# Kernel tuning notes

Hardware: AMD Instinct MI355X
Metric: run time of the kernel (lower is better)

## Reference

```python
import jax, jax.numpy as jnp
import numpy as np

BS = 64; T = 96; C = 16; IN = 16; H = 256; NH = 8; DH = H // NH
NCLS = 4; L = T + NCLS; LAYERS = 4; GDEP = 2; EPS = 1e-5


def _ln(x, g, b):
    m = x.mean(-1, keepdims=True)
    v = ((x - m) ** 2).mean(-1, keepdims=True)
    return (x - m) / jnp.sqrt(v + EPS) * g + b


def _mask():
    # causal upper-triangular -inf mask; last NCLS rows (cls tokens) attend everywhere
    m = jnp.where(jnp.triu(jnp.ones((L, L), jnp.float32), 1) > 0, -jnp.inf, 0.0)
    return m.at[-NCLS:].set(0.0)


def _enc(h, mask, Wqkv, bqkv, Wo, bo, W1, b1, W2, b2, g1, be1, g2, be2):
    # post-norm TransformerEncoderLayer (torch default), dropout=0
    B = h.shape[0]
    qkv = h @ Wqkv.T + bqkv
    q, k, v = jnp.split(qkv, 3, axis=-1)
    sp = lambda t: t.reshape(B, L, NH, DH).transpose(0, 2, 1, 3)
    q, k, v = sp(q), sp(k), sp(v)
    s = jnp.einsum('bhqd,bhkd->bhqk', q, k) / np.float32(np.sqrt(DH)) + mask
    a = jax.nn.softmax(s, axis=-1)
    o = jnp.einsum('bhqk,bhkd->bhqd', a, v).transpose(0, 2, 1, 3).reshape(B, L, H)
    h = _ln(h + o @ Wo.T + bo, g1, be1)
    ff = jax.nn.relu(h @ W1.T + b1) @ W2.T + b2
    return _ln(h + ff, g2, be2)


def _mixprop(x, g, Wm, bm):
    # x: (bs, H, C, NCLS); MTGNN mixprop with alpha=0
    adj = g + jnp.eye(C, dtype=g.dtype)
    a = adj / adj.sum(1, keepdims=True)
    h = x
    outs = [x]
    for _ in range(GDEP):
        h = jnp.einsum('ncwl,vw->ncvl', h, a)
        outs.append(h)
    ho = jnp.concatenate(outs, axis=1)  # (bs, (GDEP+1)*H, C, NCLS)
    return jnp.einsum('ncwl,oc->nowl', ho, Wm) + bm[None, :, None, None]


def _forward(x, Wfc, bfc, cls_token, pos_emb, emb1, emb2, Wl1, bl1, Wl2, bl2,
             Wqkv, bqkv, Wo, bo, W1, b1, W2, b2, ln1g, ln1b, ln2g, ln2b,
             Wmlp, bmlp, Wd1, bd1, Wd2, bd2):
    bs = x.shape[0]
    h = x @ Wfc.T + bfc                                      # (bs,T,C,H)
    h = jnp.concatenate([h, jnp.broadcast_to(cls_token, (bs, NCLS, C, H))], axis=1)
    h = h + pos_emb[None]                                    # (bs,L,C,H)
    h = jnp.swapaxes(h, 1, 2).reshape(bs * C, L, H)
    mask = _mask()
    # graph_constructor (alpha=1)
    m1 = jnp.tanh(emb1 @ Wl1.T + bl1)
    m2 = jnp.tanh(emb2 @ Wl2.T + bl2)
    g = jax.nn.relu(jnp.tanh(m1 @ m2.T - m2 @ m1.T))         # (C,C)
    h = _enc(h, mask, Wqkv[0], bqkv[0], Wo[0], bo[0], W1[0], b1[0], W2[0], b2[0],
             ln1g[0], ln1b[0], ln2g[0], ln2b[0])
    for l in range(1, LAYERS):
        cls = h[:, -NCLS:].reshape(bs, C, NCLS, H).transpose(0, 3, 1, 2)  # (bs,H,C,NCLS)
        cls = _mixprop(cls, g, Wmlp[l - 1], bmlp[l - 1])
        cls = cls.transpose(0, 2, 3, 1).reshape(bs * C, NCLS, H)
        h = jnp.concatenate([h[:, :-NCLS], cls], axis=1)
        h = _enc(h, mask, Wqkv[l], bqkv[l], Wo[l], bo[l], W1[l], b1[l], W2[l], b2[l],
                 ln1g[l], ln1b[l], ln2g[l], ln2b[l])
    z = jnp.tanh(h[:, -NCLS:].reshape(bs, C * NCLS * H))
    z = jax.nn.gelu(z @ Wd1.T + bd1, approximate=False) @ Wd2.T + bd2
    return z[:, 0]


def setup_inputs() -> dict:
    key = jax.random.key(0)
    ks = iter(jax.random.split(key, 64))
    rn = lambda *s: jax.random.normal(next(ks), s, dtype=jnp.float32) * 0.05
    d = {}
    d['x'] = jax.random.normal(next(ks), (BS, T, C, IN), dtype=jnp.float32)
    d['p'] = jnp.zeros((BS,), jnp.float32)
    d['y'] = jnp.zeros((BS,), jnp.float32)
    d['Wfc'] = rn(H, IN); d['bfc'] = jnp.zeros((H,), jnp.float32)
    d['cls_token'] = rn(1, NCLS, C, H) * 20.0  # torch randn scale ~1
    d['pos_emb'] = rn(NCLS + T, C, H) * 20.0
    d['emb1'] = rn(C, H); d['emb2'] = rn(C, H)
    d['Wl1'] = rn(H, H); d['bl1'] = jnp.zeros((H,), jnp.float32)
    d['Wl2'] = rn(H, H); d['bl2'] = jnp.zeros((H,), jnp.float32)
    d['Wqkv'] = rn(LAYERS, 3 * H, H); d['bqkv'] = jnp.zeros((LAYERS, 3 * H), jnp.float32)
    d['Wo'] = rn(LAYERS, H, H); d['bo'] = jnp.zeros((LAYERS, H), jnp.float32)
    d['W1'] = rn(LAYERS, 4 * H, H); d['b1'] = jnp.zeros((LAYERS, 4 * H), jnp.float32)
    d['W2'] = rn(LAYERS, H, 4 * H); d['b2'] = jnp.zeros((LAYERS, H), jnp.float32)
    d['ln1g'] = jnp.ones((LAYERS, H), jnp.float32); d['ln1b'] = jnp.zeros((LAYERS, H), jnp.float32)
    d['ln2g'] = jnp.ones((LAYERS, H), jnp.float32); d['ln2b'] = jnp.zeros((LAYERS, H), jnp.float32)
    d['Wmlp'] = rn(LAYERS - 1, H, (GDEP + 1) * H); d['bmlp'] = jnp.zeros((LAYERS - 1, H), jnp.float32)
    d['Wd1'] = rn(H, NCLS * C * H); d['bd1'] = jnp.zeros((H,), jnp.float32)
    d['Wd2'] = rn(1, H); d['bd2'] = jnp.zeros((1,), jnp.float32)
    return d


def reference(x, p, y, Wfc, bfc, cls_token, pos_emb, emb1, emb2, Wl1, bl1, Wl2, bl2,
              Wqkv, bqkv, Wo, bo, W1, b1, W2, b2, ln1g, ln1b, ln2g, ln2b,
              Wmlp, bmlp, Wd1, bd1, Wd2, bd2):
    # p, y are unused by the original forward (kept for signature parity)
    return _forward(x, Wfc, bfc, cls_token, pos_emb, emb1, emb2, Wl1, bl1, Wl2, bl2,
                    Wqkv, bqkv, Wo, bo, W1, b1, W2, b2, ln1g, ln1b, ln2g, ln2b,
                    Wmlp, bmlp, Wd1, bd1, Wd2, bd2)
```

## Files before the change

kernel.cpp:

```cpp
#include <hip/hip_runtime.h>
#include <hip/hip_bf16.h>
#include <math.h>

typedef unsigned short u16;
typedef unsigned int   u32;
typedef __attribute__((ext_vector_type(8))) short short8;
typedef __attribute__((ext_vector_type(4))) float f32x4;

#define BSZ   64
#define TT    96
#define CCH   16
#define INDIM 16
#define HD    256
#define NHEAD 8
#define DHEAD 32
#define NCLS  4
#define LSEQ  100
#define NLAY  4
#define EPSV  1e-5f
#define BSEQ  (BSZ*CCH)
#define MTOK  (BSEQ*LSEQ)

__device__ __forceinline__ float bf2f(u16 x){ return __uint_as_float(((u32)x)<<16); }
__device__ __forceinline__ u16 f2bf(float f){
    u32 u = __float_as_uint(f);
    u32 r = (u + 0x7fffu + ((u>>16)&1u)) >> 16;
    return (u16)r;
}
__device__ __forceinline__ float lo16(u32 r){ return __uint_as_float(r<<16); }
__device__ __forceinline__ float hi16(u32 r){ return __uint_as_float(r&0xffff0000u); }

__device__ __forceinline__ u32 cvtpk(float lo, float hi){
    u32 r;
    asm("v_cvt_pk_bf16_f32 %0, %1, %2" : "=v"(r) : "v"(lo), "v"(hi));
    return r;
}

__device__ __forceinline__ void gload_lds16(const u16* g, u16* l){
    __builtin_amdgcn_global_load_lds(
        (const __attribute__((address_space(1))) unsigned int*)g,
        (__attribute__((address_space(3))) unsigned int*)l, 16, 0, 0);
}

__global__ __launch_bounds__(256)
void k_cvt(const float* __restrict__ src, u16* __restrict__ dst, int n)
{
    for (int i = blockIdx.x*256 + threadIdx.x; i < n; i += gridDim.x*256)
        dst[i] = f2bf(src[i]);
}

__global__ __launch_bounds__(256)
void k_embed(const float* __restrict__ x, const float* __restrict__ Wfc,
             const float* __restrict__ bfc, const float* __restrict__ cls,
             const float* __restrict__ pos, u16* __restrict__ h)
{
    int s = blockIdx.x;
    int n = s >> 4, c = s & 15;
    int hc = threadIdx.x;
    float wr[INDIM];
    #pragma unroll
    for (int i=0;i<INDIM;i++) wr[i] = Wfc[hc*INDIM + i];
    float bb = bfc[hc];
    for (int l=0; l<TT; l++){
        const float* xr = x + (size_t)((n*TT + l)*CCH + c)*INDIM;
        float acc = bb;
        #pragma unroll
        for (int i=0;i<INDIM;i++) acc += xr[i]*wr[i];
        acc += pos[(size_t)(l*CCH + c)*HD + hc];
        h[((size_t)s*LSEQ + l)*HD + hc] = f2bf(acc);
    }
    #pragma unroll
    for (int l=TT; l<LSEQ; l++){
        float v = cls[(size_t)((l-TT)*CCH + c)*HD + hc]
                + pos[(size_t)(l*CCH + c)*HD + hc];
        h[((size_t)s*LSEQ + l)*HD + hc] = f2bf(v);
    }
}

__global__ __launch_bounds__(256)
void k_graph_m(const float* __restrict__ emb, const float* __restrict__ Wl,
               const float* __restrict__ bl, float* __restrict__ m)
{
    int r = blockIdx.x, o = threadIdx.x;
    __shared__ float e[HD];
    e[o] = emb[r*HD + o];
    __syncthreads();
    const float* w = Wl + (size_t)o*HD;
    float acc = bl[o];
    for (int k=0;k<HD;k++) acc += e[k]*w[k];
    m[r*HD + o] = tanhf(acc);
}

__global__ __launch_bounds__(256)
void k_graph_a(const float* __restrict__ m1, const float* __restrict__ m2,
               float* __restrict__ a)
{
    int t = threadIdx.x; int v = t >> 4, w = t & 15;
    __shared__ float adj[16][17];
    float s1=0.f, s2=0.f;
    for (int k=0;k<HD;k++){
        s1 += m1[v*HD+k]*m2[w*HD+k];
        s2 += m2[v*HD+k]*m1[w*HD+k];
    }
    float g = tanhf(s1 - s2); g = g > 0.f ? g : 0.f;
    adj[v][w] = g + (v==w ? 1.f : 0.f);
    __syncthreads();
    float rs = 0.f;
    #pragma unroll
    for (int j=0;j<16;j++) rs += adj[v][j];
    a[t] = adj[v][w] / rs;
}

__global__ __launch_bounds__(256)
void k_gemmA(const u16* __restrict__ A, int lda,
             const u16* __restrict__ W, const float* __restrict__ bias,
             u16* __restrict__ C, int ldc, int K, int relu, int scat)
{
    __shared__ u16 As0[2][128*32], As1[2][128*32];
    __shared__ u16 Ws0[2][128*32], Ws1[2][128*32];
    int t = threadIdx.x;
    int lane = t & 63, w = t >> 6;
    int wm = (w & 1)*64, wn = (w >> 1)*64;
    int fr = lane & 15, quad = lane >> 4;
    size_t mb = (size_t)blockIdx.x * 128;
    int nb = blockIdx.y * 128;
    int srow = lane >> 2;
    int sslot = lane & 3;

    f32x4 acc[4][4] = {};

    auto STAGE = [&](int bb, int k0){
        #pragma unroll
        for (int i=0;i<2;i++){
            int r = w*32 + i*16 + srow;
            int cw = sslot ^ ((r>>1)&3);
            gload_lds16(&A[(mb + r)*(size_t)lda + k0      + cw*8], &As0[bb][(w*32 + i*16)*32]);
            gload_lds16(&A[(mb + r)*(size_t)lda + k0 + 32 + cw*8], &As1[bb][(w*32 + i*16)*32]);
            gload_lds16(&W[(size_t)(nb + r)*K   + k0      + cw*8], &Ws0[bb][(w*32 + i*16)*32]);
            gload_lds16(&W[(size_t)(nb + r)*K   + k0 + 32 + cw*8], &Ws1[bb][(w*32 + i*16)*32]);
        }
    };
    auto COMPUTE = [&](int bb){
        short8 af0[4], af1[4], bf0[4], bf1[4];
        #pragma unroll
        for (int mt=0; mt<4; mt++){
            int r = wm + mt*16 + fr;
            int sw = (quad ^ ((r>>1)&3)) << 3;
            af0[mt] = *(const short8*)&As0[bb][r*32 + sw];
            af1[mt] = *(const short8*)&As1[bb][r*32 + sw];
        }
        #pragma unroll
        for (int nt=0; nt<4; nt++){
            int r = wn + nt*16 + fr;
            int sw = (quad ^ ((r>>1)&3)) << 3;
            bf0[nt] = *(const short8*)&Ws0[bb][r*32 + sw];
            bf1[nt] = *(const short8*)&Ws1[bb][r*32 + sw];
        }
        #pragma unroll
        for (int mt=0; mt<4; mt++)
            #pragma unroll
            for (int nt=0; nt<4; nt++){
                acc[mt][nt] = __builtin_amdgcn_mfma_f32_16x16x32_bf16(
                    af0[mt], bf0[nt], acc[mt][nt], 0, 0, 0);
                acc[mt][nt] = __builtin_amdgcn_mfma_f32_16x16x32_bf16(
                    af1[mt], bf1[nt], acc[mt][nt], 0, 0, 0);
            }
    };

    const int nst = K >> 6;
    STAGE(0, 0);
    asm volatile("s_waitcnt vmcnt(0)" ::: "memory");
    __builtin_amdgcn_s_barrier();
    int b = 0;
    for (int ts = 0; ts < nst; ++ts){
        if (ts + 1 < nst) STAGE(b^1, (ts+1) << 6);
        COMPUTE(b);
        asm volatile("s_waitcnt vmcnt(0)" ::: "memory");
        __builtin_amdgcn_s_barrier();
        b ^= 1;
    }

    float bb4[4];
    #pragma unroll
    for (int nt=0; nt<4; nt++) bb4[nt] = bias[nb + wn + nt*16 + fr];
    #pragma unroll
    for (int mt=0; mt<4; mt++){
        size_t rbase = mb + wm + mt*16 + quad*4;
        size_t rows[4];
        #pragma unroll
        for (int r=0; r<4; r++){
            size_t rg = rbase + r;
            if (scat) rg = (rg >> 2)*LSEQ + TT + (rg & 3);
            rows[r] = rg*(size_t)ldc;
        }
        #pragma unroll
        for (int nt=0; nt<4; nt++){
            int col = nb + wn + nt*16 + fr;
            float v0 = acc[mt][nt][0] + bb4[nt];
            float v1 = acc[mt][nt][1] + bb4[nt];
            float v2 = acc[mt][nt][2] + bb4[nt];
            float v3 = acc[mt][nt][3] + bb4[nt];
            if (relu){
                v0 = v0 > 0.f ? v0 : 0.f;  v1 = v1 > 0.f ? v1 : 0.f;
                v2 = v2 > 0.f ? v2 : 0.f;  v3 = v3 > 0.f ? v3 : 0.f;
            }
            u32 p01 = cvtpk(v0, v1), p23 = cvtpk(v2, v3);
            C[rows[0] + col] = (u16)p01;
            C[rows[1] + col] = (u16)(p01 >> 16);
            C[rows[2] + col] = (u16)p23;
            C[rows[3] + col] = (u16)(p23 >> 16);
        }
    }
}

__global__ __launch_bounds__(256)
void k_gemmC(const u16* __restrict__ A, int lda, int K,
             const u16* __restrict__ W, const float* __restrict__ bias,
             u16* __restrict__ h, const float* __restrict__ gam,
             const float* __restrict__ bet, size_t row0)
{
    __shared__ u16 As0[2][64*32], As1[2][64*32];
    __shared__ u16 Ws0[2][256*32], Ws1[2][256*32];
    int t = threadIdx.x;
    int lane = t & 63, w = t >> 6;
    int fr = lane & 15, quad = lane >> 4;
    size_t mb = (size_t)blockIdx.x * 64;
    int srow = lane >> 2, sslot = lane & 3;

    f32x4 acc[4][4] = {};

    auto STAGE = [&](int bb, int k0){
        {
            int r = w*16 + srow;
            int cw = sslot ^ ((r>>1)&3);
            gload_lds16(&A[(mb + r)*(size_t)lda + k0      + cw*8], &As0[bb][(w*16)*32]);
            gload_lds16(&A[(mb + r)*(size_t)lda + k0 + 32 + cw*8], &As1[bb][(w*16)*32]);
        }
        #pragma unroll
        for (int i=0;i<4;i++){
            int r = w*64 + i*16 + srow;
            int cw = sslot ^ ((r>>1)&3);
            gload_lds16(&W[(size_t)r*K + k0      + cw*8], &Ws0[bb][(w*64 + i*16)*32]);
            gload_lds16(&W[(size_t)r*K + k0 + 32 + cw*8], &Ws1[bb][(w*64 + i*16)*32]);
        }
    };
    auto COMPUTE = [&](int bb){
        short8 af0[4], af1[4], bf0[4], bf1[4];
        #pragma unroll
        for (int mt=0; mt<4; mt++){
            int ra = mt*16 + fr;
            int swa = (quad ^ ((ra>>1)&3)) << 3;
            af0[mt] = *(const short8*)&As0[bb][ra*32 + swa];
            af1[mt] = *(const short8*)&As1[bb][ra*32 + swa];
        }
        #pragma unroll
        for (int nt=0; nt<4; nt++){
            int rb = w*64 + nt*16 + fr;
            int swb = (quad ^ ((rb>>1)&3)) << 3;
            bf0[nt] = *(const short8*)&Ws0[bb][rb*32 + swb];
            bf1[nt] = *(const short8*)&Ws1[bb][rb*32 + swb];
        }
        #pragma unroll
        for (int mt=0; mt<4; mt++)
            #pragma unroll
            for (int nt=0; nt<4; nt++){
                acc[mt][nt] = __builtin_amdgcn_mfma_f32_16x16x32_bf16(
                    af0[mt], bf0[nt], acc[mt][nt], 0, 0, 0);
                acc[mt][nt] = __builtin_amdgcn_mfma_f32_16x16x32_bf16(
                    af1[mt], bf1[nt], acc[mt][nt], 0, 0, 0);
            }
    };

    const int nst = K >> 6;
    STAGE(0, 0);
    asm volatile("s_waitcnt vmcnt(0)" ::: "memory");
    __builtin_amdgcn_s_barrier();
    int b = 0;
    for (int ts = 0; ts < nst; ++ts){
        if (ts + 1 < nst) STAGE(b^1, (ts+1) << 6);
        COMPUTE(b);
        asm volatile("s_waitcnt vmcnt(0)" ::: "memory");
        __builtin_amdgcn_s_barrier();
        b ^= 1;
    }

    float bb4[4], gg[4], be[4];
    #pragma unroll
    for (int nt=0; nt<4; nt++){
        int col = w*64 + nt*16 + fr;
        bb4[nt] = bias[col]; gg[nt] = gam[col]; be[nt] = bet[col];
    }
    #pragma unroll
    for (int mt=0; mt<4; mt++){
        #pragma unroll
        for (int r=0; r<4; r++){
            size_t row = row0 + mb + mt*16 + quad*4 + r;
            #pragma unroll
            for (int nt=0; nt<4; nt++)
                acc[mt][nt][r] += bb4[nt] + bf2f(h[row*HD + w*64 + nt*16 + fr]);
        }
    }
    __syncthreads();
    float* red  = (float*)As0;
    float* red2 = (float*)As1;
    float ps[4][4];
    #pragma unroll
    for (int mt=0; mt<4; mt++)
        #pragma unroll
        for (int r=0; r<4; r++){
            float s = acc[mt][0][r] + acc[mt][1][r] + acc[mt][2][r] + acc[mt][3][r];
            s += __shfl_xor(s,1,64); s += __shfl_xor(s,2,64);
            s += __shfl_xor(s,4,64); s += __shfl_xor(s,8,64);
            ps[mt][r] = s;
        }
    if (fr == 0){
        #pragma unroll
        for (int mt=0; mt<4; mt++)
            #pragma unroll
            for (int r=0; r<4; r++)
                red[w*64 + mt*16 + quad*4 + r] = ps[mt][r];
    }
    __syncthreads();
    float mean[4][4];
    #pragma unroll
    for (int mt=0; mt<4; mt++)
        #pragma unroll
        for (int r=0; r<4; r++){
            int rl = mt*16 + quad*4 + r;
            mean[mt][r] = (red[rl] + red[64+rl] + red[128+rl] + red[192+rl]) * (1.f/256.f);
            float s = 0.f;
            #pragma unroll
            for (int nt=0; nt<4; nt++){ float d = acc[mt][nt][r] - mean[mt][r]; s += d*d; }
            s += __shfl_xor(s,1,64); s += __shfl_xor(s,2,64);
            s += __shfl_xor(s,4,64); s += __shfl_xor(s,8,64);
            ps[mt][r] = s;
        }
    if (fr == 0){
        #pragma unroll
        for (int mt=0; mt<4; mt++)
            #pragma unroll
            for (int r=0; r<4; r++)
                red2[w*64 + mt*16 + quad*4 + r] = ps[mt][r];
    }
    __syncthreads();
    #pragma unroll
    for (int mt=0; mt<4; mt++)
        #pragma unroll
        for (int r=0; r<4; r++){
            int rl = mt*16 + quad*4 + r;
            float inv = rsqrtf((red2[rl] + red2[64+rl] + red2[128+rl] + red2[192+rl])
                               * (1.f/256.f) + EPSV);
            size_t row = row0 + mb + rl;
            float o0 = (acc[mt][0][r] - mean[mt][r]) * inv * gg[0] + be[0];
            float o1 = (acc[mt][1][r] - mean[mt][r]) * inv * gg[1] + be[1];
            float o2 = (acc[mt][2][r] - mean[mt][r]) * inv * gg[2] + be[2];
            float o3 = (acc[mt][3][r] - mean[mt][r]) * inv * gg[3] + be[3];
            u32 p01 = cvtpk(o0, o1), p23 = cvtpk(o2, o3);
            h[row*HD + w*64 +  0 + fr] = (u16)p01;
            h[row*HD + w*64 + 16 + fr] = (u16)(p01 >> 16);
            h[row*HD + w*64 + 32 + fr] = (u16)p23;
            h[row*HD + w*64 + 48 + fr] = (u16)(p23 >> 16);
        }
}

#define KS_STR 40
#define VT_STR 136
#define PL_STR 136
__global__ __launch_bounds__(256)
void k_attn(u16* __restrict__ qkv)
{
    __shared__ u16 smem[26368];
    int t = threadIdx.x;
    int w = t >> 6, lane = t & 63;
    int fr = lane & 15, quad = lane >> 4;
    int p = t >> 7, t2 = t & 127;
    u16* Ks = smem + p*4480;
    u16* Vt = smem + 8960 + p*4352;
    u16* Pl = smem + 17664 + w*2176;

    {
        int gp = blockIdx.x*2 + p;
        size_t base = (size_t)(gp >> 3)*LSEQ*768 + (gp & 7)*32;
        for (int idx = t2; idx < 1792; idx += 128){
            int key = idx >> 4, d2 = (idx & 15) << 1;
            u32 kv = (key < LSEQ) ? *(const u32*)&qkv[base + (size_t)key*768 + 256 + d2] : 0u;
            *(u32*)&Ks[key*KS_STR + d2] = kv;
        }
        for (int idx = t2; idx < 2048; idx += 128){
            int key = idx >> 4, d2 = (idx & 15) << 1;
            u32 vv = (key < LSEQ) ? *(const u32*)&qkv[base + (size_t)key*768 + 512 + d2] : 0u;
            Vt[ d2   *VT_STR + key] = (u16)(vv & 0xffffu);
            Vt[(d2+1)*VT_STR + key] = (u16)(vv >> 16);
        }
    }
    __syncthreads();

    int wp = w >> 1;
    int gp = blockIdx.x*2 + wp;
    size_t base = (size_t)(gp >> 3)*LSEQ*768 + (gp & 7)*32;
    u16* Ksw = smem + wp*4480;
    u16* Vtw = smem + 8960 + wp*4352;

    short8 kf[7];
    #pragma unroll
    for (int nt=0; nt<7; nt++)
        kf[nt] = *(const short8*)&Ksw[(nt*16 + fr)*KS_STR + quad*8];
    short8 vfr[4][2];
    #pragma unroll
    for (int ks=0; ks<4; ks++)
        #pragma unroll
        for (int nt=0; nt<2; nt++)
            vfr[ks][nt] = *(const short8*)&Vtw[(nt*16 + fr)*VT_STR + ks*32 + quad*8];

    const float scale = 0.17677669529663687f;
    int smask = (w & 1) ? 0x34 : 0x4B;
    #pragma unroll
    for (int st = 0; st < 7; ++st){
        if (!((smask >> st) & 1)) continue;
        const int ntile = (st == 6) ? 7 : (st + 1);
        const int nks   = (st == 6) ? 4 : (st/2 + 1);
        int q = st*16 + fr;
        short8 qf = {};
        if (q < LSEQ) qf = *(const short8*)&qkv[base + (size_t)q*768 + quad*8];
        f32x4 S[7];
        #pragma unroll
        for (int nt=0; nt<7; nt++){
            if (nt >= ntile) continue;
            f32x4 z = {};
            S[nt] = __builtin_amdgcn_mfma_f32_16x16x32_bf16(qf, kf[nt], z, 0,0,0);
        }
        float mx[4] = {-1e30f,-1e30f,-1e30f,-1e30f};
        #pragma unroll
        for (int r=0;r<4;r++){
            int qr = st*16 + quad*4 + r;
            int jmax = (qr < TT) ? qr : (LSEQ-1);
            #pragma unroll
            for (int nt=0;nt<7;nt++){
                if (nt >= ntile) continue;
                int j = nt*16 + fr;
                float s = (j <= jmax) ? S[nt][r]*scale : -1e30f;
                S[nt][r] = s;
                mx[r] = fmaxf(mx[r], s);
            }
        }
        #pragma unroll
        for (int r=0;r<4;r++){
            #pragma unroll
            for (int m=1;m<16;m<<=1) mx[r] = fmaxf(mx[r], __shfl_xor(mx[r], m, 64));
        }
        float l4[4] = {0.f,0.f,0.f,0.f};
        #pragma unroll
        for (int r=0;r<4;r++){
            #pragma unroll
            for (int nt=0;nt<7;nt++){
                if (nt >= ntile) continue;
                float pv = __expf(S[nt][r] - mx[r]);
                S[nt][r] = pv;
                l4[r] += pv;
            }
        }
        #pragma unroll
        for (int r=0;r<4;r++){
            #pragma unroll
            for (int m=1;m<16;m<<=1) l4[r] += __shfl_xor(l4[r], m, 64);
        }
        #pragma unroll
        for (int nt=0;nt<7;nt++){
            if (nt >= ntile) continue;
            #pragma unroll
            for (int r=0;r<4;r++){
                u16 hb = f2bf(S[nt][r]);
                Pl[(quad*4+r)*PL_STR + nt*16 + fr] = hb;
                S[nt][r] -= bf2f(hb);
            }
        }
        if (ntile*16 < nks*32){
            #pragma unroll
            for (int r=0;r<4;r++)
                Pl[(quad*4+r)*PL_STR + ntile*16 + fr] = 0;
        }
        __builtin_amdgcn_s_waitcnt(0);
        f32x4 D[2] = {};
        #pragma unroll
        for (int ks=0; ks<4; ks++){
            if (ks >= nks) continue;
            short8 pf = *(const short8*)&Pl[fr*PL_STR + ks*32 + quad*8];
            #pragma unroll
            for (int nt=0; nt<2; nt++)
                D[nt] = __builtin_amdgcn_mfma_f32_16x16x32_bf16(pf, vfr[ks][nt], D[nt], 0,0,0);
        }
        __builtin_amdgcn_s_waitcnt(0);
        #pragma unroll
        for (int nt=0;nt<7;nt++){
            if (nt >= ntile) continue;
            #pragma unroll
            for (int r=0;r<4;r++)
                Pl[(quad*4+r)*PL_STR + nt*16 + fr] = f2bf(S[nt][r]);
        }
        __builtin_amdgcn_s_waitcnt(0);
        #pragma unroll
        for (int ks=0; ks<4; ks++){
            if (ks >= nks) continue;
            short8 pf = *(const short8*)&Pl[fr*PL_STR + ks*32 + quad*8];
            #pragma unroll
            for (int nt=0; nt<2; nt++)
                D[nt] = __builtin_amdgcn_mfma_f32_16x16x32_bf16(pf, vfr[ks][nt], D[nt], 0,0,0);
        }
        #pragma unroll
        for (int r=0;r<4;r++){
            int qr = st*16 + quad*4 + r;
            if (qr < LSEQ){
                float inv = 1.f / l4[r];
                #pragma unroll
                for (int nt=0; nt<2; nt++)
                    qkv[base + (size_t)qr*768 + nt*16 + fr] = f2bf(D[nt][r]*inv);
            }
        }
        __builtin_amdgcn_s_waitcnt(0);
    }
}

__global__ __launch_bounds__(256)
void k_mixprep(const u16* __restrict__ h, const float* __restrict__ a,
               u16* __restrict__ amid)
{
    int n = blockIdx.x >> 2, tt = blockIdx.x & 3;
    __shared__ float xs[256][17], h1s[256][17], h2s[256][17];
    __shared__ float as[16][17];
    int t = threadIdx.x;
    as[t>>4][t&15] = a[t];
    for (int idx=t; idx<4096; idx+=256){
        int w = idx >> 8, hc = idx & 255;
        xs[hc][w] = bf2f(h[((size_t)(n*16 + w)*LSEQ + TT + tt)*HD + hc]);
    }
    __syncthreads();
    for (int idx=t; idx<4096; idx+=256){
        int v = idx & 15, hc = idx >> 4;
        float acc = 0.f;
        #pragma unroll
        for (int w=0;w<16;w++) acc += as[v][w]*xs[hc][w];
        h1s[hc][v] = acc;
    }
    __syncthreads();
    for (int idx=t; idx<4096; idx+=256){
        int v = idx & 15, hc = idx >> 4;
        float acc = 0.f;
        #pragma unroll
        for (int w=0;w<16;w++) acc += as[v][w]*h1s[hc][w];
        h2s[hc][v] = acc;
    }
    __syncthreads();
    int hc = t;
    #pragma unroll
    for (int w=0;w<16;w++){
        size_t row = (size_t)((n*16 + w)*4 + tt);
        amid[row*768 +       hc] = f2bf(xs[hc][w]);
        amid[row*768 + 256 + hc] = f2bf(h1s[hc][w]);
        amid[row*768 + 512 + hc] = f2bf(h2s[hc][w]);
    }
}

__global__ __launch_bounds__(256)
void k_z(const u16* __restrict__ h, u16* __restrict__ z)
{
    int bid = blockIdx.x, t = threadIdx.x;
    #pragma unroll
    for (int tc=0;tc<4;tc++)
        z[((size_t)bid*4 + tc)*HD + t] = f2bf(tanhf(bf2f(h[((size_t)bid*LSEQ + TT + tc)*HD + t])));
}

__global__ __launch_bounds__(256)
void k_head1p(const u16* __restrict__ z, const float* __restrict__ Wd1,
              float* __restrict__ d1p)
{
    __shared__ float zch[64][137];
    __shared__ float wt[16][137];
    int t = threadIdx.x;
    int col = t & 15, rgrp = t >> 4;
    int ob = blockIdx.x * 16;
    int kb = blockIdx.y;
    float acc[4] = {0.f,0.f,0.f,0.f};
    for (int kc=0; kc<1024; kc+=128){
        int base_k = kb*1024 + kc;
        #pragma unroll
        for (int jj=0; jj<16; jj++){
            int idx = t + jj*256;
            int n = idx >> 6, k2 = (idx & 63) << 1;
            u32 r = *(const u32*)&z[(size_t)n*16384 + base_k + k2];
            zch[n][k2] = lo16(r); zch[n][k2+1] = hi16(r);
        }
        #pragma unroll
        for (int jj=0; jj<2; jj++){
            int idx = t + jj*256;
            int r = idx >> 5, k4 = (idx & 31) << 2;
            float4 w4 = *(const float4*)&Wd1[(size_t)(ob + r)*16384 + base_k + k4];
            wt[r][k4] = w4.x; wt[r][k4+1] = w4.y; wt[r][k4+2] = w4.z; wt[r][k4+3] = w4.w;
        }
        __syncthreads();
        for (int k=0;k<128;k++){
            float wv = wt[col][k];
            #pragma unroll
            for (int u=0;u<4;u++) acc[u] += zch[rgrp + 16*u][k]*wv;
        }
        __syncthreads();
    }
    #pragma unroll
    for (int u=0;u<4;u++)
        d1p[(size_t)(kb*64 + rgrp + 16*u)*HD + ob + col] = acc[u];
}

__global__ __launch_bounds__(256)
void k_headf(const float* __restrict__ d1p, const float* __restrict__ bd1,
             const float* __restrict__ Wd2, const float* __restrict__ bd2,
             float* __restrict__ out)
{
    __shared__ float red[4];
    int n = blockIdx.x, c = threadIdx.x;
    float s = 0.f;
    #pragma unroll
    for (int kb=0; kb<16; kb++) s += d1p[(size_t)(kb*64 + n)*HD + c];
    float xx = s + bd1[c];
    float ge = 0.5f*xx*(1.f + erff(xx*0.70710678118654752f));
    float p = ge * Wd2[c];
    #pragma unroll
    for (int m=1;m<64;m<<=1) p += __shfl_xor(p, m, 64);
    if ((c & 63) == 0) red[c >> 6] = p;
    __syncthreads();
    if (c == 0) out[n] = red[0]+red[1]+red[2]+red[3] + bd2[0];
}

extern "C" void kernel_launch(void* const* d_in, const int* in_sizes, int n_in,
                              void* d_out, int out_size, void* d_ws, size_t ws_size,
                              hipStream_t stream)
{
    const float* x    = (const float*)d_in[0];
    const float* Wfc  = (const float*)d_in[3];
    const float* bfc  = (const float*)d_in[4];
    const float* cls  = (const float*)d_in[5];
    const float* pos  = (const float*)d_in[6];
    const float* emb1 = (const float*)d_in[7];
    const float* emb2 = (const float*)d_in[8];
    const float* Wl1  = (const float*)d_in[9];
    const float* bl1  = (const float*)d_in[10];
    const float* Wl2  = (const float*)d_in[11];
    const float* bl2  = (const float*)d_in[12];
    const float* Wqkv = (const float*)d_in[13];
    const float* bqkv = (const float*)d_in[14];
    const float* Wo   = (const float*)d_in[15];
    const float* bo   = (const float*)d_in[16];
    const float* W1   = (const float*)d_in[17];
    const float* b1   = (const float*)d_in[18];
    const float* W2   = (const float*)d_in[19];
    const float* b2   = (const float*)d_in[20];
    const float* ln1g = (const float*)d_in[21];
    const float* ln1b = (const float*)d_in[22];
    const float* ln2g = (const float*)d_in[23];
    const float* ln2b = (const float*)d_in[24];
    const float* Wmlp = (const float*)d_in[25];
    const float* bmlp = (const float*)d_in[26];
    const float* Wd1  = (const float*)d_in[27];
    const float* bd1  = (const float*)d_in[28];
    const float* Wd2  = (const float*)d_in[29];
    const float* bd2  = (const float*)d_in[30];

    int NCH = 8;
    {
        const size_t fixed = 63145088 + (1<<20);
        if      (fixed + (size_t)MTOK    *2560 <= ws_size) NCH = 1;
        else if (fixed + (size_t)(MTOK/2)*2560 <= ws_size) NCH = 2;
        else if (fixed + (size_t)(MTOK/4)*2560 <= ws_size) NCH = 4;
    }
    const int RCH = MTOK / NCH;
    const int SCH = BSEQ / NCH;

    u16* h    = (u16*)d_ws;
    u16* buf  = h    + (size_t)MTOK*HD;
    u16* buf2 = buf  + (size_t)RCH*1024;
    u16* wq   = buf2 + (size_t)RCH*256;
    u16* wo   = wq   + (size_t)4*768*256;
    u16* w1   = wo   + (size_t)4*256*256;
    u16* w2   = w1   + (size_t)4*1024*256;
    u16* wmb  = w2   + (size_t)4*256*1024;
    u16* zb   = wmb  + (size_t)3*256*768;
    float* fp = (float*)(zb + (size_t)BSZ*16384);
    float* m1  = fp;
    float* m2  = m1 + CCH*HD;
    float* an  = m2 + CCH*HD;
    float* d1p = an + CCH*CCH;

    k_cvt<<<512, 256, 0, stream>>>(Wqkv, wq, 4*768*256);
    k_cvt<<<256, 256, 0, stream>>>(Wo,   wo, 4*256*256);
    k_cvt<<<512, 256, 0, stream>>>(W1,   w1, 4*1024*256);
    k_cvt<<<512, 256, 0, stream>>>(W2,   w2, 4*256*1024);
    k_cvt<<<256, 256, 0, stream>>>(Wmlp, wmb, 3*256*768);

    k_embed<<<BSEQ, 256, 0, stream>>>(x, Wfc, bfc, cls, pos, h);
    k_graph_m<<<16, 256, 0, stream>>>(emb1, Wl1, bl1, m1);
    k_graph_m<<<16, 256, 0, stream>>>(emb2, Wl2, bl2, m2);
    k_graph_a<<<1, 256, 0, stream>>>(m1, m2, an);

    for (int l=0; l<NLAY; l++){
        if (l > 0){
            k_mixprep<<<BSZ*NCLS, 256, 0, stream>>>(h, an, buf);
            k_gemmA<<<dim3(4096/128, 256/128), 256, 0, stream>>>(
                buf, 768, wmb + (size_t)(l-1)*256*768, bmlp + (size_t)(l-1)*HD,
                h, HD, 768, 0, 1);
        }

        for (int c=0; c<NCH; c++){
            size_t row0 = (size_t)c * RCH;
            k_gemmA<<<dim3(RCH/128, 768/128), 256, 0, stream>>>(
                h + row0*HD, HD, wq + (size_t)l*768*256, bqkv + (size_t)l*768,
                buf, 768, HD, 0, 0);
            k_attn<<<SCH*NHEAD/2, 256, 0, stream>>>(buf);
            k_gemmC<<<RCH/64, 256, 0, stream>>>(
                buf, 768, HD, wo + (size_t)l*256*256, bo + (size_t)l*HD,
                h, ln1g + (size_t)l*HD, ln1b + (size_t)l*HD, row0);
            k_gemmA<<<dim3(RCH/128, 1024/128), 256, 0, stream>>>(
                h + row0*HD, HD, w1 + (size_t)l*1024*256, b1 + (size_t)l*1024,
                buf, 1024, HD, 1, 0);
            k_gemmC<<<RCH/64, 256, 0, stream>>>(
                buf, 1024, 1024, w2 + (size_t)l*256*1024, b2 + (size_t)l*HD,
                h, ln2g + (size_t)l*HD, ln2b + (size_t)l*HD, row0);
        }
    }

    k_z<<<BSZ*CCH, 256, 0, stream>>>(h, zb);
    k_head1p<<<dim3(16, 16), 256, 0, stream>>>(zb, Wd1, d1p);
    k_headf<<<BSZ, 256, 0, stream>>>(d1p, bd1, Wd2, bd2, (float*)d_out);
}
```

Before: 2.257 ms.

## Fuse FFN up-projection, ReLU, down-projection and LayerNorm into one kernel

Replaces the separate W1 GEMM (writing a 1024-wide intermediate to global memory) and the W2+residual+LayerNorm GEMM with a single kernel per 64-row tile. The kernel keeps the input rows in LDS, computes 256-column chunks of the ReLU intermediate into LDS, and accumulates the down-projection in registers, streaming double-buffered weight tiles. This removes the global round trip of the FFN intermediate and one launch, at the cost of heavy LDS use (about 96KB per block) and lower occupancy, with weights reloaded by every block.

```diff
diff --git a/kernel.cpp b/kernel.cpp
--- a/kernel.cpp
+++ b/kernel.cpp
@@ -355,6 +355,232 @@
             float o1 = (acc[mt][1][r] - mean[mt][r]) * inv * gg[1] + be[1];
             float o2 = (acc[mt][2][r] - mean[mt][r]) * inv * gg[2] + be[2];
             float o3 = (acc[mt][3][r] - mean[mt][r]) * inv * gg[3] + be[3];
+            u32 p01 = cvtpk(o0, o1), p23 = cvtpk(o2, o3);
+            h[row*HD + w*64 +  0 + fr] = (u16)p01;
+            h[row*HD + w*64 + 16 + fr] = (u16)(p01 >> 16);
+            h[row*HD + w*64 + 32 + fr] = (u16)p23;
+            h[row*HD + w*64 + 48 + fr] = (u16)(p23 >> 16);
+        }
+}
+
+__global__ __launch_bounds__(256)
+void k_ffn(const u16* __restrict__ W1, const float* __restrict__ b1,
+           const u16* __restrict__ W2, const float* __restrict__ b2v,
+           u16* __restrict__ h, const float* __restrict__ gam,
+           const float* __restrict__ bet, size_t row0)
+{
+    __shared__ u16 Ah0[4][64*32], Ah1[4][64*32];
+    __shared__ u16 F10[4][64*32], F11[4][64*32];
+    __shared__ u16 Ws0[2][256*32], Ws1[2][256*32];
+    int t = threadIdx.x;
+    int lane = t & 63, w = t >> 6;
+    int fr = lane & 15, quad = lane >> 4;
+    size_t mb = (size_t)blockIdx.x * 64;
+    int srow = lane >> 2, sslot = lane & 3;
+
+    f32x4 acc2[4][4] = {};
+
+    {
+        #pragma unroll
+        for (int i=0;i<4;i++){
+            int r = i*16 + srow;
+            int cw = sslot ^ ((r>>1)&3);
+            gload_lds16(&h[(row0 + mb + r)*HD + w*64      + cw*8], &Ah0[w][(i*16)*32]);
+            gload_lds16(&h[(row0 + mb + r)*HD + w*64 + 32 + cw*8], &Ah1[w][(i*16)*32]);
+        }
+    }
+    auto STAGE_W1 = [&](int bb, int n1, int kk){
+        const u16* Wp = W1 + (size_t)(n1*256)*HD;
+        #pragma unroll
+        for (int i=0;i<4;i++){
+            int r = w*64 + i*16 + srow;
+            int cw = sslot ^ ((r>>1)&3);
+            gload_lds16(&Wp[(size_t)r*HD + kk*64      + cw*8], &Ws0[bb][(w*64 + i*16)*32]);
+            gload_lds16(&Wp[(size_t)r*HD + kk*64 + 32 + cw*8], &Ws1[bb][(w*64 + i*16)*32]);
+        }
+    };
+    auto STAGE_W2 = [&](int bb, int n1, int kk){
+        #pragma unroll
+        for (int i=0;i<4;i++){
+            int r = w*64 + i*16 + srow;
+            int cw = sslot ^ ((r>>1)&3);
+            gload_lds16(&W2[(size_t)r*1024 + n1*256 + kk*64      + cw*8], &Ws0[bb][(w*64 + i*16)*32]);
+            gload_lds16(&W2[(size_t)r*1024 + n1*256 + kk*64 + 32 + cw*8], &Ws1[bb][(w*64 + i*16)*32]);
+        }
+    };
+
+    STAGE_W1(0, 0, 0);
+    asm volatile("s_waitcnt vmcnt(0)" ::: "memory");
+    __builtin_amdgcn_s_barrier();
+    int bb = 0;
+
+    for (int n1 = 0; n1 < 4; ++n1){
+        f32x4 acc1[4][4] = {};
+        float b1c[4];
+        #pragma unroll
+        for (int nt=0; nt<4; nt++) b1c[nt] = b1[n1*256 + w*64 + nt*16 + fr];
+
+        for (int kk = 0; kk < 4; ++kk){
+            if (kk < 3) STAGE_W1(bb^1, n1, kk+1);
+            else        STAGE_W2(bb^1, n1, 0);
+            short8 af0[4], af1[4], bf0[4], bf1[4];
+            #pragma unroll
+            for (int mt=0; mt<4; mt++){
+                int ra = mt*16 + fr;
+                int swa = (quad ^ ((ra>>1)&3)) << 3;
+                af0[mt] = *(const short8*)&Ah0[kk][ra*32 + swa];
+                af1[mt] = *(const short8*)&Ah1[kk][ra*32 + swa];
+            }
+            #pragma unroll
+            for (int nt=0; nt<4; nt++){
+                int rb = w*64 + nt*16 + fr;
+                int swb = (quad ^ ((rb>>1)&3)) << 3;
+                bf0[nt] = *(const short8*)&Ws0[bb][rb*32 + swb];
+                bf1[nt] = *(const short8*)&Ws1[bb][rb*32 + swb];
+            }
+            #pragma unroll
+            for (int mt=0; mt<4; mt++)
+                #pragma unroll
+                for (int nt=0; nt<4; nt++){
+                    acc1[mt][nt] = __builtin_amdgcn_mfma_f32_16x16x32_bf16(
+                        af0[mt], bf0[nt], acc1[mt][nt], 0, 0, 0);
+                    acc1[mt][nt] = __builtin_amdgcn_mfma_f32_16x16x32_bf16(
+                        af1[mt], bf1[nt], acc1[mt][nt], 0, 0, 0);
+                }
+            asm volatile("s_waitcnt vmcnt(0)" ::: "memory");
+            __builtin_amdgcn_s_barrier();
+            bb ^= 1;
+        }
+
+        #pragma unroll
+        for (int mt=0; mt<4; mt++){
+            #pragma unroll
+            for (int r=0; r<4; r++){
+                int row = mt*16 + quad*4 + r;
+                int s_ = (row>>1)&3;
+                #pragma unroll
+                for (int nt=0; nt<4; nt++){
+                    float v = acc1[mt][nt][r] + b1c[nt];
+                    v = v > 0.f ? v : 0.f;
+                    u16 hv = f2bf(v);
+                    int g = ((nt&1)*2 + (fr>>3)) ^ s_;
+                    if (nt < 2) F10[w][row*32 + g*8 + (fr&7)] = hv;
+                    else        F11[w][row*32 + g*8 + (fr&7)] = hv;
+                }
+            }
+        }
+        asm volatile("s_waitcnt lgkmcnt(0)" ::: "memory");
+        __builtin_amdgcn_s_barrier();
+
+        for (int kk = 0; kk < 4; ++kk){
+            if (kk < 3)      STAGE_W2(bb^1, n1, kk+1);
+            else if (n1 < 3) STAGE_W1(bb^1, n1+1, 0);
+            short8 af0[4], af1[4], bf0[4], bf1[4];
+            #pragma unroll
+            for (int mt=0; mt<4; mt++){
+                int ra = mt*16 + fr;
+                int swa = (quad ^ ((ra>>1)&3)) << 3;
+                af0[mt] = *(const short8*)&F10[kk][ra*32 + swa];
+                af1[mt] = *(const short8*)&F11[kk][ra*32 + swa];
+            }
+            #pragma unroll
+            for (int nt=0; nt<4; nt++){
+                int rb = w*64 + nt*16 + fr;
+                int swb = (quad ^ ((rb>>1)&3)) << 3;
+                bf0[nt] = *(const short8*)&Ws0[bb][rb*32 + swb];
+                bf1[nt] = *(const short8*)&Ws1[bb][rb*32 + swb];
+            }
+            #pragma unroll
+            for (int mt=0; mt<4; mt++)
+                #pragma unroll
+                for (int nt=0; nt<4; nt++){
+                    acc2[mt][nt] = __builtin_amdgcn_mfma_f32_16x16x32_bf16(
+                        af0[mt], bf0[nt], acc2[mt][nt], 0, 0, 0);
+                    acc2[mt][nt] = __builtin_amdgcn_mfma_f32_16x16x32_bf16(
+                        af1[mt], bf1[nt], acc2[mt][nt], 0, 0, 0);
+                }
+            asm volatile("s_waitcnt vmcnt(0)" ::: "memory");
+            __builtin_amdgcn_s_barrier();
+            bb ^= 1;
+        }
+    }
+
+    float bb4[4], gg[4], be[4];
+    #pragma unroll
+    for (int nt=0; nt<4; nt++){
+        int col = w*64 + nt*16 + fr;
+        bb4[nt] = b2v[col]; gg[nt] = gam[col]; be[nt] = bet[col];
+    }
+    #pragma unroll
+    for (int mt=0; mt<4; mt++){
+        #pragma unroll
+        for (int r=0; r<4; r++){
+            int row = mt*16 + quad*4 + r;
+            int s_ = (row>>1)&3;
+            #pragma unroll
+            for (int nt=0; nt<4; nt++){
+                int g = ((nt&1)*2 + (fr>>3)) ^ s_;
+                u16 rv = (nt < 2) ? Ah0[w][row*32 + g*8 + (fr&7)]
+                                  : Ah1[w][row*32 + g*8 + (fr&7)];
+                acc2[mt][nt][r] += bb4[nt] + bf2f(rv);
+            }
+        }
+    }
+    __syncthreads();
+    float* red  = (float*)Ws0;
+    float* red2 = (float*)Ws1;
+    float ps[4][4];
+    #pragma unroll
+    for (int mt=0; mt<4; mt++)
+        #pragma unroll
+        for (int r=0; r<4; r++){
+            float s = acc2[mt][0][r] + acc2[mt][1][r] + acc2[mt][2][r] + acc2[mt][3][r];
+            s += __shfl_xor(s,1,64); s += __shfl_xor(s,2,64);
+            s += __shfl_xor(s,4,64); s += __shfl_xor(s,8,64);
+            ps[mt][r] = s;
+        }
+    if (fr == 0){
+        #pragma unroll
+        for (int mt=0; mt<4; mt++)
+            #pragma unroll
+            for (int r=0; r<4; r++)
+                red[w*64 + mt*16 + quad*4 + r] = ps[mt][r];
+    }
+    __syncthreads();
+    float mean[4][4];
+    #pragma unroll
+    for (int mt=0; mt<4; mt++)
+        #pragma unroll
+        for (int r=0; r<4; r++){
+            int rl = mt*16 + quad*4 + r;
+            mean[mt][r] = (red[rl] + red[64+rl] + red[128+rl] + red[192+rl]) * (1.f/256.f);
+            float s = 0.f;
+            #pragma unroll
+            for (int nt=0; nt<4; nt++){ float d = acc2[mt][nt][r] - mean[mt][r]; s += d*d; }
+            s += __shfl_xor(s,1,64); s += __shfl_xor(s,2,64);
+            s += __shfl_xor(s,4,64); s += __shfl_xor(s,8,64);
+            ps[mt][r] = s;
+        }
+    if (fr == 0){
+        #pragma unroll
+        for (int mt=0; mt<4; mt++)
+            #pragma unroll
+            for (int r=0; r<4; r++)
+                red2[w*64 + mt*16 + quad*4 + r] = ps[mt][r];
+    }
+    __syncthreads();
+    #pragma unroll
+    for (int mt=0; mt<4; mt++)
+        #pragma unroll
+        for (int r=0; r<4; r++){
+            int rl = mt*16 + quad*4 + r;
+            float inv = rsqrtf((red2[rl] + red2[64+rl] + red2[128+rl] + red2[192+rl])
+                               * (1.f/256.f) + EPSV);
+            size_t row = row0 + mb + rl;
+            float o0 = (acc2[mt][0][r] - mean[mt][r]) * inv * gg[0] + be[0];
+            float o1 = (acc2[mt][1][r] - mean[mt][r]) * inv * gg[1] + be[1];
+            float o2 = (acc2[mt][2][r] - mean[mt][r]) * inv * gg[2] + be[2];
+            float o3 = (acc2[mt][3][r] - mean[mt][r]) * inv * gg[3] + be[3];
             u32 p01 = cvtpk(o0, o1), p23 = cvtpk(o2, o3);
             h[row*HD + w*64 +  0 + fr] = (u16)p01;
             h[row*HD + w*64 + 16 + fr] = (u16)(p01 >> 16);
@@ -716,11 +942,9 @@
             k_gemmC<<<RCH/64, 256, 0, stream>>>(
                 buf, 768, HD, wo + (size_t)l*256*256, bo + (size_t)l*HD,
                 h, ln1g + (size_t)l*HD, ln1b + (size_t)l*HD, row0);
-            k_gemmA<<<dim3(RCH/128, 1024/128), 256, 0, stream>>>(
-                h + row0*HD, HD, w1 + (size_t)l*1024*256, b1 + (size_t)l*1024,
-                buf, 1024, HD, 1, 0);
-            k_gemmC<<<RCH/64, 256, 0, stream>>>(
-                buf, 1024, 1024, w2 + (size_t)l*256*1024, b2 + (size_t)l*HD,
+            k_ffn<<<RCH/64, 256, 0, stream>>>(
+                w1 + (size_t)l*1024*256, b1 + (size_t)l*1024,
+                w2 + (size_t)l*256*1024, b2 + (size_t)l*HD,
                 h, ln2g + (size_t)l*HD, ln2b + (size_t)l*HD, row0);
         }
     }
```

New measurement: 2.398 ms. +6.2%, slower.

## Stage GEMM epilogues through LDS for coalesced stores and remap tiles per XCD

Applied to the files above, without the earlier changes.

Both GEMM kernels now write their bf16 results into shared memory first and then store them to global memory as 16-byte row-contiguous vectors, replacing scattered 2-byte stores. k_gemmA also remaps block ids so consecutive tiles land on the same XCD (stride-8 interleave), with the grid swapped so N tiles vary fastest, to improve L2 reuse of A rows. This costs extra barriers and an LDS round trip in the epilogue, and the shared buffers are unified so they can be reused.

```diff
diff --git a/kernel.cpp b/kernel.cpp
--- a/kernel.cpp
+++ b/kernel.cpp
@@ -116,14 +116,28 @@
              const u16* __restrict__ W, const float* __restrict__ bias,
              u16* __restrict__ C, int ldc, int K, int relu, int scat)
 {
-    __shared__ u16 As0[2][128*32], As1[2][128*32];
-    __shared__ u16 Ws0[2][128*32], Ws1[2][128*32];
+    __shared__ u16 smem[32768];
+    u16* As0 = smem;
+    u16* As1 = smem + 8192;
+    u16* Ws0 = smem + 16384;
+    u16* Ws1 = smem + 24576;
+
     int t = threadIdx.x;
     int lane = t & 63, w = t >> 6;
     int wm = (w & 1)*64, wn = (w >> 1)*64;
     int fr = lane & 15, quad = lane >> 4;
-    size_t mb = (size_t)blockIdx.x * 128;
-    int nb = blockIdx.y * 128;
+
+    int nwg = gridDim.x * gridDim.y;
+    int bid = blockIdx.y * gridDim.x + blockIdx.x;
+    int tile = bid;
+    if (!(nwg & 7)){
+        int cpx = nwg >> 3;
+        tile = (bid & 7)*cpx + (bid >> 3);
+    }
+    int bx = tile % gridDim.x, by = tile / gridDim.x;
+    size_t mb = (size_t)by * 128;
+    int nb = bx * 128;
+
     int srow = lane >> 2;
     int sslot = lane & 3;
 
@@ -134,10 +148,10 @@
         for (int i=0;i<2;i++){
             int r = w*32 + i*16 + srow;
             int cw = sslot ^ ((r>>1)&3);
-            gload_lds16(&A[(mb + r)*(size_t)lda + k0      + cw*8], &As0[bb][(w*32 + i*16)*32]);
-            gload_lds16(&A[(mb + r)*(size_t)lda + k0 + 32 + cw*8], &As1[bb][(w*32 + i*16)*32]);
-            gload_lds16(&W[(size_t)(nb + r)*K   + k0      + cw*8], &Ws0[bb][(w*32 + i*16)*32]);
-            gload_lds16(&W[(size_t)(nb + r)*K   + k0 + 32 + cw*8], &Ws1[bb][(w*32 + i*16)*32]);
+            gload_lds16(&A[(mb + r)*(size_t)lda + k0      + cw*8], &As0[bb*4096 + (w*32 + i*16)*32]);
+            gload_lds16(&A[(mb + r)*(size_t)lda + k0 + 32 + cw*8], &As1[bb*4096 + (w*32 + i*16)*32]);
+            gload_lds16(&W[(size_t)(nb + r)*K   + k0      + cw*8], &Ws0[bb*4096 + (w*32 + i*16)*32]);
+            gload_lds16(&W[(size_t)(nb + r)*K   + k0 + 32 + cw*8], &Ws1[bb*4096 + (w*32 + i*16)*32]);
         }
     };
     auto COMPUTE = [&](int bb){
@@ -146,15 +160,15 @@
         for (int mt=0; mt<4; mt++){
             int r = wm + mt*16 + fr;
             int sw = (quad ^ ((r>>1)&3)) << 3;
-            af0[mt] = *(const short8*)&As0[bb][r*32 + sw];
-            af1[mt] = *(const short8*)&As1[bb][r*32 + sw];
+            af0[mt] = *(const short8*)&As0[bb*4096 + r*32 + sw];
+            af1[mt] = *(const short8*)&As1[bb*4096 + r*32 + sw];
         }
         #pragma unroll
         for (int nt=0; nt<4; nt++){
             int r = wn + nt*16 + fr;
             int sw = (quad ^ ((r>>1)&3)) << 3;
-            bf0[nt] = *(const short8*)&Ws0[bb][r*32 + sw];
-            bf1[nt] = *(const short8*)&Ws1[bb][r*32 + sw];
+            bf0[nt] = *(const short8*)&Ws0[bb*4096 + r*32 + sw];
+            bf1[nt] = *(const short8*)&Ws1[bb*4096 + r*32 + sw];
         }
         #pragma unroll
         for (int mt=0; mt<4; mt++)
@@ -183,19 +197,14 @@
     float bb4[4];
     #pragma unroll
     for (int nt=0; nt<4; nt++) bb4[nt] = bias[nb + wn + nt*16 + fr];
+    __syncthreads();
+    u16* Ct = smem;
     #pragma unroll
     for (int mt=0; mt<4; mt++){
-        size_t rbase = mb + wm + mt*16 + quad*4;
-        size_t rows[4];
-        #pragma unroll
-        for (int r=0; r<4; r++){
-            size_t rg = rbase + r;
-            if (scat) rg = (rg >> 2)*LSEQ + TT + (rg & 3);
-            rows[r] = rg*(size_t)ldc;
-        }
+        int rw = wm + mt*16 + quad*4;
         #pragma unroll
         for (int nt=0; nt<4; nt++){
-            int col = nb + wn + nt*16 + fr;
+            int col = wn + nt*16 + fr;
             float v0 = acc[mt][nt][0] + bb4[nt];
             float v1 = acc[mt][nt][1] + bb4[nt];
             float v2 = acc[mt][nt][2] + bb4[nt];
@@ -205,11 +214,20 @@
                 v2 = v2 > 0.f ? v2 : 0.f;  v3 = v3 > 0.f ? v3 : 0.f;
             }
             u32 p01 = cvtpk(v0, v1), p23 = cvtpk(v2, v3);
-            C[rows[0] + col] = (u16)p01;
-            C[rows[1] + col] = (u16)(p01 >> 16);
-            C[rows[2] + col] = (u16)p23;
-            C[rows[3] + col] = (u16)(p23 >> 16);
-        }
+            Ct[(rw+0)*128 + col] = (u16)p01;
+            Ct[(rw+1)*128 + col] = (u16)(p01 >> 16);
+            Ct[(rw+2)*128 + col] = (u16)p23;
+            Ct[(rw+3)*128 + col] = (u16)(p23 >> 16);
+        }
+    }
+    __syncthreads();
+    #pragma unroll
+    for (int it=0; it<8; ++it){
+        int row = it*16 + (t>>4);
+        int seg = t & 15;
+        size_t rg = mb + row;
+        if (scat) rg = (rg >> 2)*LSEQ + TT + (rg & 3);
+        *(short8*)&C[rg*(size_t)ldc + nb + seg*8] = *(const short8*)&Ct[row*128 + seg*8];
     }
 }
 
@@ -219,8 +237,12 @@
              u16* __restrict__ h, const float* __restrict__ gam,
              const float* __restrict__ bet, size_t row0)
 {
-    __shared__ u16 As0[2][64*32], As1[2][64*32];
-    __shared__ u16 Ws0[2][256*32], Ws1[2][256*32];
+    __shared__ u16 smem[40960];
+    u16* As0 = smem;
+    u16* As1 = smem + 4096;
+    u16* Ws0 = smem + 8192;
+    u16* Ws1 = smem + 24576;
+
     int t = threadIdx.x;
     int lane = t & 63, w = t >> 6;
     int fr = lane & 15, quad = lane >> 4;
@@ -233,15 +255,15 @@
         {
             int r = w*16 + srow;
             int cw = sslot ^ ((r>>1)&3);
-            gload_lds16(&A[(mb + r)*(size_t)lda + k0      + cw*8], &As0[bb][(w*16)*32]);
-            gload_lds16(&A[(mb + r)*(size_t)lda + k0 + 32 + cw*8], &As1[bb][(w*16)*32]);
+            gload_lds16(&A[(mb + r)*(size_t)lda + k0      + cw*8], &As0[bb*2048 + (w*16)*32]);
+            gload_lds16(&A[(mb + r)*(size_t)lda + k0 + 32 + cw*8], &As1[bb*2048 + (w*16)*32]);
         }
         #pragma unroll
         for (int i=0;i<4;i++){
             int r = w*64 + i*16 + srow;
             int cw = sslot ^ ((r>>1)&3);
-            gload_lds16(&W[(size_t)r*K + k0      + cw*8], &Ws0[bb][(w*64 + i*16)*32]);
-            gload_lds16(&W[(size_t)r*K + k0 + 32 + cw*8], &Ws1[bb][(w*64 + i*16)*32]);
+            gload_lds16(&W[(size_t)r*K + k0      + cw*8], &Ws0[bb*8192 + (w*64 + i*16)*32]);
+            gload_lds16(&W[(size_t)r*K + k0 + 32 + cw*8], &Ws1[bb*8192 + (w*64 + i*16)*32]);
         }
     };
     auto COMPUTE = [&](int bb){
@@ -250,15 +272,15 @@
         for (int mt=0; mt<4; mt++){
             int ra = mt*16 + fr;
             int swa = (quad ^ ((ra>>1)&3)) << 3;
-            af0[mt] = *(const short8*)&As0[bb][ra*32 + swa];
-            af1[mt] = *(const short8*)&As1[bb][ra*32 + swa];
+            af0[mt] = *(const short8*)&As0[bb*2048 + ra*32 + swa];
+            af1[mt] = *(const short8*)&As1[bb*2048 + ra*32 + swa];
         }
         #pragma unroll
         for (int nt=0; nt<4; nt++){
             int rb = w*64 + nt*16 + fr;
             int swb = (quad ^ ((rb>>1)&3)) << 3;
-            bf0[nt] = *(const short8*)&Ws0[bb][rb*32 + swb];
-            bf1[nt] = *(const short8*)&Ws1[bb][rb*32 + swb];
+            bf0[nt] = *(const short8*)&Ws0[bb*8192 + rb*32 + swb];
+            bf1[nt] = *(const short8*)&Ws1[bb*8192 + rb*32 + swb];
         }
         #pragma unroll
         for (int mt=0; mt<4; mt++)
@@ -301,8 +323,8 @@
         }
     }
     __syncthreads();
-    float* red  = (float*)As0;
-    float* red2 = (float*)As1;
+    float* red  = (float*)smem;
+    float* red2 = (float*)(smem + 512);
     float ps[4][4];
     #pragma unroll
     for (int mt=0; mt<4; mt++)
@@ -343,6 +365,7 @@
                 red2[w*64 + mt*16 + quad*4 + r] = ps[mt][r];
     }
     __syncthreads();
+    u16* Ct = smem + 8192;
     #pragma unroll
     for (int mt=0; mt<4; mt++)
         #pragma unroll
@@ -350,17 +373,23 @@
             int rl = mt*16 + quad*4 + r;
             float inv = rsqrtf((red2[rl] + red2[64+rl] + red2[128+rl] + red2[192+rl])
                                * (1.f/256.f) + EPSV);
-            size_t row = row0 + mb + rl;
             float o0 = (acc[mt][0][r] - mean[mt][r]) * inv * gg[0] + be[0];
             float o1 = (acc[mt][1][r] - mean[mt][r]) * inv * gg[1] + be[1];
             float o2 = (acc[mt][2][r] - mean[mt][r]) * inv * gg[2] + be[2];
             float o3 = (acc[mt][3][r] - mean[mt][r]) * inv * gg[3] + be[3];
             u32 p01 = cvtpk(o0, o1), p23 = cvtpk(o2, o3);
-            h[row*HD + w*64 +  0 + fr] = (u16)p01;
-            h[row*HD + w*64 + 16 + fr] = (u16)(p01 >> 16);
-            h[row*HD + w*64 + 32 + fr] = (u16)p23;
-            h[row*HD + w*64 + 48 + fr] = (u16)(p23 >> 16);
-        }
+            Ct[rl*256 + w*64 +  0 + fr] = (u16)p01;
+            Ct[rl*256 + w*64 + 16 + fr] = (u16)(p01 >> 16);
+            Ct[rl*256 + w*64 + 32 + fr] = (u16)p23;
+            Ct[rl*256 + w*64 + 48 + fr] = (u16)(p23 >> 16);
+        }
+    __syncthreads();
+    #pragma unroll
+    for (int it=0; it<8; ++it){
+        int row = it*8 + (t>>5);
+        int seg = t & 31;
+        *(short8*)&h[(row0 + mb + row)*HD + seg*8] = *(const short8*)&Ct[row*256 + seg*8];
+    }
 }
 
 #define KS_STR 40
@@ -702,21 +731,21 @@
     for (int l=0; l<NLAY; l++){
         if (l > 0){
             k_mixprep<<<BSZ*NCLS, 256, 0, stream>>>(h, an, buf);
-            k_gemmA<<<dim3(4096/128, 256/128), 256, 0, stream>>>(
+            k_gemmA<<<dim3(256/128, 4096/128), 256, 0, stream>>>(
                 buf, 768, wmb + (size_t)(l-1)*256*768, bmlp + (size_t)(l-1)*HD,
                 h, HD, 768, 0, 1);
         }
 
         for (int c=0; c<NCH; c++){
             size_t row0 = (size_t)c * RCH;
-            k_gemmA<<<dim3(RCH/128, 768/128), 256, 0, stream>>>(
+            k_gemmA<<<dim3(768/128, RCH/128), 256, 0, stream>>>(
                 h + row0*HD, HD, wq + (size_t)l*768*256, bqkv + (size_t)l*768,
                 buf, 768, HD, 0, 0);
             k_attn<<<SCH*NHEAD/2, 256, 0, stream>>>(buf);
             k_gemmC<<<RCH/64, 256, 0, stream>>>(
                 buf, 768, HD, wo + (size_t)l*256*256, bo + (size_t)l*HD,
                 h, ln1g + (size_t)l*HD, ln1b + (size_t)l*HD, row0);
-            k_gemmA<<<dim3(RCH/128, 1024/128), 256, 0, stream>>>(
+            k_gemmA<<<dim3(1024/128, RCH/128), 256, 0, stream>>>(
                 h + row0*HD, HD, w1 + (size_t)l*1024*256, b1 + (size_t)l*1024,
                 buf, 1024, HD, 1, 0);
             k_gemmC<<<RCH/64, 256, 0, stream>>>(
```

Result: faster. 2.104 ms (-6.8%).
